# Optimization experiments

Hardware: AMD Instinct MI355X
Metric: run time of the kernel (lower is better)

The kernel has to match this reference:

```python
import jax, jax.numpy as jnp
import numpy as np
import itertools

RANK = 2  # window size per axis; mode='linear' -> stride 1; rank_op='avg'; rank_mode='drop'


def setup_inputs() -> dict:
    key = jax.random.key(0)
    k1, k2, k3 = jax.random.split(key, 3)
    m = 32
    D = 20
    hypervol = jax.random.normal(k1, (D, D, D, D, m), dtype=jnp.float32)
    # nn.Linear weight init U(-0.5, 0.5); P init U(-0.1, 0.1)
    M_w = jax.random.uniform(k2, (m, m), dtype=jnp.float32, minval=-0.5, maxval=0.5)
    P = jax.random.uniform(k3, (m, m), dtype=jnp.float32, minval=-0.1, maxval=0.1)
    return {"hypervol": hypervol, "M_w": M_w, "P": P}


def reference(hypervol, M_w, P):
    m = P.shape[0]
    D1, D2, D3, D4, _ = hypervol.shape
    o1, o2, o3, o4 = D1 - RANK + 1, D2 - RANK + 1, D3 - RANK + 1, D4 - RANK + 1

    # Vectorized window extraction with mean reduction ('avg'):
    # mean over RANK^4 window = average of RANK^4 shifted slices (fixed small loop).
    acc = jnp.zeros((o1, o2, o3, o4, m), dtype=hypervol.dtype)
    for a, b, c, d in itertools.product(range(RANK), repeat=4):
        acc = acc + hypervol[a:a + o1, b:b + o2, c:c + o3, d:d + o4, :]
    win = acc / float(RANK ** 4)  # [o1,o2,o3,o4,m]

    # M(v): Linear without bias -> v @ W^T
    x = jnp.einsum('abcdj,ij->abcdi', win, M_w)  # [o1,o2,o3,o4,m]
    # note: output index of Linear is i; below x plays role of (M v) with einsum index j
    x = jnp.einsum('abcdi->abcdi', x)  # no-op, keep shape clear

    # periods[i,j] = i*m + j + 2 (identical for all four axes)
    ii = jnp.arange(m, dtype=jnp.float32)
    periods = ii[:, None] * m + ii[None, :] + 2.0  # [m,m]
    two_pi = jnp.float32(2.0 * np.pi)

    def ctab(n):
        k = jnp.arange(n, dtype=jnp.float32)
        return jnp.cos(two_pi * k[:, None, None] / periods)  # [n,m,m]

    C1, C2, C3, C4 = ctab(o1), ctab(o2), ctab(o3), ctab(o4)
    # phi[a,b,c,d,i,j] = C1[a]*C2[b]*C3[c]*C4[d]; built from tiny per-axis tables
    phi = (C1[:, None, None, None] * C2[None, :, None, None]) \
          [:, :, :, None] * 0.0  # placeholder removed below
    phi = (C1[:, None, None, None, :, :]
           * C2[None, :, None, None, :, :]
           * C3[None, None, :, None, :, :]
           * C4[None, None, None, :, :, :])  # [o1,o2,o3,o4,m,m]

    # N(k)_i = sum_j P_ij * (Mv)_j * phi_ij  (matches einsum 'bj,ij,bij->bi')
    Nk = jnp.einsum('abcdj,ij,abcdij->abcdi', x, P, phi)
    return Nk.reshape(-1, m)  # [num_windows, m], window order = k1-major like the loops
```

## Files before the change

### kernel.cpp

```cpp
#include <hip/hip_runtime.h>

#define DD 20
#define MM 32
#define OO 19
#define NWIN (OO*OO*OO)
#define WPB 4
#define NBLK ((NWIN + WPB - 1) / WPB)

#define CT_FLOATS (OO*MM*MM)
#define PT_OFF CT_FLOATS
#define MT_OFF (PT_OFF + MM*MM)
#define WS_FLOATS (MT_OFF + MM*MM)

__global__ __launch_bounds__(256) void build_tables_kernel(
        const float* __restrict__ Mw, const float* __restrict__ P,
        float* __restrict__ ws) {
    int idx = blockIdx.x * 256 + threadIdx.x;
    if (idx < CT_FLOATS) {
        int k = idx >> 10;
        int r = idx & 1023;
        int j = r >> 5;
        int i = r & 31;
        float period = (float)(i * MM + j + 2);
        ws[idx] = cosf(6.28318530717958647692f * (float)k / period);
    } else if (idx < MT_OFF) {
        int r = idx - PT_OFF;
        ws[idx] = P[(r & 31) * MM + (r >> 5)];
    } else if (idx < WS_FLOATS) {
        int r = idx - MT_OFF;
        ws[idx] = Mw[(r & 31) * MM + (r >> 5)];
    }
}

__device__ __forceinline__ void wave_sync() {
    __builtin_amdgcn_s_waitcnt(0);
    __builtin_amdgcn_wave_barrier();
}

__global__ __launch_bounds__(256, 4) void spatial_kernel(
        const float* __restrict__ H, const float* __restrict__ ws,
        float* __restrict__ out) {
    __shared__ __align__(16) float sS[WPB][DD * MM];
    __shared__ __align__(16) float sW[WPB][OO * MM];
    __shared__ __align__(16) float sX[WPB][OO * MM];

    const int tid  = threadIdx.x;
    const int w    = tid >> 6;
    const int lane = tid & 63;
    const int i    = lane & 31;
    const int h    = lane >> 5;
    const int jb   = h * 16;

    const int raw = blockIdx.x;
    const int xcd = raw & 7;
    const int k   = raw >> 3;
    const int sb  = (xcd < 3) ? (xcd * 215 + k) : (645 + (xcd - 3) * 214 + k);
    const int win = sb * WPB + w;
    if (win >= NWIN) return;
    const int c = win % OO;
    const int b = (win / OO) % OO;
    const int a = win / (OO * OO);

    const float* __restrict__ Ct = ws;
    const float* __restrict__ Pt = ws + PT_OFF;
    const float* __restrict__ Mt = ws + MT_OFF;

    float* __restrict__ S = sS[w];
    float* __restrict__ W = sW[w];
    float* __restrict__ X = sX[w];

    {
        float2 acc[5];
        #pragma unroll
        for (int kk = 0; kk < 5; ++kk) acc[kk] = make_float2(0.f, 0.f);
        #pragma unroll
        for (int da = 0; da < 2; ++da)
            #pragma unroll
            for (int db = 0; db < 2; ++db)
                #pragma unroll
                for (int dc = 0; dc < 2; ++dc) {
                    const float2* __restrict__ p = (const float2*)(
                        H + (size_t)((((a + da) * DD + (b + db)) * DD + (c + dc)) * DD) * MM);
                    #pragma unroll
                    for (int kk = 0; kk < 5; ++kk) {
                        const float2 v = p[kk * 64 + lane];
                        acc[kk].x += v.x; acc[kk].y += v.y;
                    }
                }
        #pragma unroll
        for (int kk = 0; kk < 5; ++kk)
            ((float2*)S)[kk * 64 + lane] = acc[kk];
    }
    wave_sync();

    #pragma unroll
    for (int t = 0; t < 10; ++t) {
        const int idx = t * 64 + lane;
        if (idx < OO * MM)
            W[idx] = (S[idx] + S[idx + MM]) * 0.0625f;
    }
    wave_sync();

    {
        float mt[16];
        #pragma unroll
        for (int jj = 0; jj < 16; ++jj)
            mt[jj] = Mt[(jb + jj) * MM + i];

        #pragma unroll
        for (int d = 0; d < OO; ++d) {
            const float4* __restrict__ wr = (const float4*)(W + d * MM + jb);
            float t = 0.f;
            #pragma unroll
            for (int q = 0; q < 4; ++q) {
                const float4 v = wr[q];
                t += v.x * mt[q*4+0] + v.y * mt[q*4+1]
                   + v.z * mt[q*4+2] + v.w * mt[q*4+3];
            }
            t += __shfl_xor(t, 32, 64);
            if (h == 0) X[d * MM + i] = t;
        }
    }
    wave_sync();

    float s0[16], s1[16], t2c[16];
    {
        const float* __restrict__ cta = Ct + a * (MM * MM);
        const float* __restrict__ ctb = Ct + b * (MM * MM);
        const float* __restrict__ ctc = Ct + c * (MM * MM);
        const float* __restrict__ ct1 = Ct + 1 * (MM * MM);
        #pragma unroll
        for (int jj = 0; jj < 16; ++jj) {
            const int o = (jb + jj) * MM + i;
            const float qp  = Pt[o] * cta[o] * ctb[o] * ctc[o];
            const float cw  = ct1[o];
            t2c[jj] = cw + cw;
            s1[jj]  = qp;
            s0[jj]  = qp * cw;
        }
    }
    const size_t obase = (size_t)win * (OO * MM);
    #pragma unroll
    for (int d = 0; d < OO; ++d) {
        const float4* __restrict__ xr = (const float4*)(X + d * MM + jb);
        float t = 0.f;
        #pragma unroll
        for (int q = 0; q < 4; ++q) {
            const float4 v = xr[q];
            t += v.x * s1[q*4+0] + v.y * s1[q*4+1]
               + v.z * s1[q*4+2] + v.w * s1[q*4+3];
        }
        #pragma unroll
        for (int jj = 0; jj < 16; ++jj) {
            const float nx = __builtin_fmaf(t2c[jj], s1[jj], -s0[jj]);
            s0[jj] = s1[jj];
            s1[jj] = nx;
        }
        t += __shfl_xor(t, 32, 64);
        if (h == 0) out[obase + d * MM + i] = t;
    }
}

extern "C" void kernel_launch(void* const* d_in, const int* in_sizes, int n_in,
                              void* d_out, int out_size, void* d_ws, size_t ws_size,
                              hipStream_t stream) {
    const float* H  = (const float*)d_in[0];
    const float* Mw = (const float*)d_in[1];
    const float* P  = (const float*)d_in[2];
    float* out = (float*)d_out;
    float* ws  = (float*)d_ws;

    const int tblocks = (WS_FLOATS + 255) / 256;
    build_tables_kernel<<<tblocks, 256, 0, stream>>>(Mw, P, ws);
    spatial_kernel<<<NBLK, 256, 0, stream>>>(H, ws, out);
}
```

Baseline: 94.78 us.

## Split spatial kernel into two stages with global intermediate and vectorized loads

Splits the fused kernel into stage1 (window averaging plus the M projection, written to a global workspace) and stage2 (the cosine-recurrence contraction with P, read back from global). Each stage uses less LDS and fewer registers, so more waves can be resident per CU. The cos table layout is transposed so P, M and the tables are read with contiguous float4 loads directly instead of through pre-transposed copies. The price is an extra kernel launch and an intermediate array of about 26 MB written and read through global memory, and the LDS sync now waits only on LDS counters.

Result: slower. 134.3 us (+41.8%).

```diff
diff --git a/kernel.cpp b/kernel.cpp
--- a/kernel.cpp
+++ b/kernel.cpp
@@ -8,41 +8,38 @@
 #define NBLK ((NWIN + WPB - 1) / WPB)
 
 #define CT_FLOATS (OO*MM*MM)
-#define PT_OFF CT_FLOATS
-#define MT_OFF (PT_OFF + MM*MM)
-#define WS_FLOATS (MT_OFF + MM*MM)
+#define XOFF CT_FLOATS
+#define XROW (OO*MM)
 
-__global__ __launch_bounds__(256) void build_tables_kernel(
-        const float* __restrict__ Mw, const float* __restrict__ P,
-        float* __restrict__ ws) {
+__global__ __launch_bounds__(256) void build_tables_kernel(float* __restrict__ ws) {
     int idx = blockIdx.x * 256 + threadIdx.x;
     if (idx < CT_FLOATS) {
         int k = idx >> 10;
         int r = idx & 1023;
-        int j = r >> 5;
-        int i = r & 31;
+        int i = r >> 5;
+        int j = r & 31;
         float period = (float)(i * MM + j + 2);
         ws[idx] = cosf(6.28318530717958647692f * (float)k / period);
-    } else if (idx < MT_OFF) {
-        int r = idx - PT_OFF;
-        ws[idx] = P[(r & 31) * MM + (r >> 5)];
-    } else if (idx < WS_FLOATS) {
-        int r = idx - MT_OFF;
-        ws[idx] = Mw[(r & 31) * MM + (r >> 5)];
     }
 }
 
-__device__ __forceinline__ void wave_sync() {
-    __builtin_amdgcn_s_waitcnt(0);
+__device__ __forceinline__ void lds_sync() {
+    __builtin_amdgcn_s_waitcnt(0xC07F);
     __builtin_amdgcn_wave_barrier();
 }
 
-__global__ __launch_bounds__(256, 4) void spatial_kernel(
-        const float* __restrict__ H, const float* __restrict__ ws,
-        float* __restrict__ out) {
+__device__ __forceinline__ int swizzled_win(int raw, int w) {
+    const int xcd = raw & 7;
+    const int k   = raw >> 3;
+    const int sb  = (xcd < 3) ? (xcd * 215 + k) : (645 + (xcd - 3) * 214 + k);
+    return sb * WPB + w;
+}
+
+__global__ __launch_bounds__(256, 8) void stage1_kernel(
+        const float* __restrict__ H, const float* __restrict__ Mw,
+        float* __restrict__ ws) {
     __shared__ __align__(16) float sS[WPB][DD * MM];
     __shared__ __align__(16) float sW[WPB][OO * MM];
-    __shared__ __align__(16) float sX[WPB][OO * MM];
 
     const int tid  = threadIdx.x;
     const int w    = tid >> 6;
@@ -51,47 +48,40 @@
     const int h    = lane >> 5;
     const int jb   = h * 16;
 
-    const int raw = blockIdx.x;
-    const int xcd = raw & 7;
-    const int k   = raw >> 3;
-    const int sb  = (xcd < 3) ? (xcd * 215 + k) : (645 + (xcd - 3) * 214 + k);
-    const int win = sb * WPB + w;
+    const int win = swizzled_win(blockIdx.x, w);
     if (win >= NWIN) return;
     const int c = win % OO;
     const int b = (win / OO) % OO;
     const int a = win / (OO * OO);
 
-    const float* __restrict__ Ct = ws;
-    const float* __restrict__ Pt = ws + PT_OFF;
-    const float* __restrict__ Mt = ws + MT_OFF;
-
     float* __restrict__ S = sS[w];
     float* __restrict__ W = sW[w];
-    float* __restrict__ X = sX[w];
 
     {
-        float2 acc[5];
-        #pragma unroll
-        for (int kk = 0; kk < 5; ++kk) acc[kk] = make_float2(0.f, 0.f);
+        float4 a0 = make_float4(0.f,0.f,0.f,0.f);
+        float4 a1 = a0, a2 = a0;
         #pragma unroll
         for (int da = 0; da < 2; ++da)
             #pragma unroll
             for (int db = 0; db < 2; ++db)
                 #pragma unroll
                 for (int dc = 0; dc < 2; ++dc) {
-                    const float2* __restrict__ p = (const float2*)(
+                    const float4* __restrict__ p = (const float4*)(
                         H + (size_t)((((a + da) * DD + (b + db)) * DD + (c + dc)) * DD) * MM);
-                    #pragma unroll
-                    for (int kk = 0; kk < 5; ++kk) {
-                        const float2 v = p[kk * 64 + lane];
-                        acc[kk].x += v.x; acc[kk].y += v.y;
+                    float4 v0 = p[lane];
+                    float4 v1 = p[64 + lane];
+                    a0.x += v0.x; a0.y += v0.y; a0.z += v0.z; a0.w += v0.w;
+                    a1.x += v1.x; a1.y += v1.y; a1.z += v1.z; a1.w += v1.w;
+                    if (lane < 32) {
+                        float4 v2 = p[128 + lane];
+                        a2.x += v2.x; a2.y += v2.y; a2.z += v2.z; a2.w += v2.w;
                     }
                 }
-        #pragma unroll
-        for (int kk = 0; kk < 5; ++kk)
-            ((float2*)S)[kk * 64 + lane] = acc[kk];
+        ((float4*)S)[lane]      = a0;
+        ((float4*)S)[64 + lane] = a1;
+        if (lane < 32) ((float4*)S)[128 + lane] = a2;
     }
-    wave_sync();
+    lds_sync();
 
     #pragma unroll
     for (int t = 0; t < 10; ++t) {
@@ -99,14 +89,16 @@
         if (idx < OO * MM)
             W[idx] = (S[idx] + S[idx + MM]) * 0.0625f;
     }
-    wave_sync();
+    lds_sync();
 
     {
         float mt[16];
         #pragma unroll
-        for (int jj = 0; jj < 16; ++jj)
-            mt[jj] = Mt[(jb + jj) * MM + i];
-
+        for (int q = 0; q < 4; ++q) {
+            const float4 v = ((const float4*)(Mw + i * MM + jb))[q];
+            mt[q*4+0] = v.x; mt[q*4+1] = v.y; mt[q*4+2] = v.z; mt[q*4+3] = v.w;
+        }
+        float* __restrict__ Xg = ws + XOFF + (size_t)win * XROW;
         #pragma unroll
         for (int d = 0; d < OO; ++d) {
             const float4* __restrict__ wr = (const float4*)(W + d * MM + jb);
@@ -118,35 +110,58 @@
                    + v.z * mt[q*4+2] + v.w * mt[q*4+3];
             }
             t += __shfl_xor(t, 32, 64);
-            if (h == 0) X[d * MM + i] = t;
+            if (h == 0) Xg[d * MM + i] = t;
         }
     }
-    wave_sync();
+}
+
+__global__ __launch_bounds__(256, 6) void stage2_kernel(
+        const float* __restrict__ ws, const float* __restrict__ P,
+        float* __restrict__ out) {
+    const int tid  = threadIdx.x;
+    const int w    = tid >> 6;
+    const int lane = tid & 63;
+    const int i    = lane & 31;
+    const int h    = lane >> 5;
+    const int jb   = h * 16;
+
+    const int win = swizzled_win(blockIdx.x, w);
+    if (win >= NWIN) return;
+    const int c = win % OO;
+    const int b = (win / OO) % OO;
+    const int a = win / (OO * OO);
+
+    const float* __restrict__ C = ws;
 
     float s0[16], s1[16], t2c[16];
     {
-        const float* __restrict__ cta = Ct + a * (MM * MM);
-        const float* __restrict__ ctb = Ct + b * (MM * MM);
-        const float* __restrict__ ctc = Ct + c * (MM * MM);
-        const float* __restrict__ ct1 = Ct + 1 * (MM * MM);
+        const int ro = i * MM + jb;
         #pragma unroll
-        for (int jj = 0; jj < 16; ++jj) {
-            const int o = (jb + jj) * MM + i;
-            const float qp  = Pt[o] * cta[o] * ctb[o] * ctc[o];
-            const float cw  = ct1[o];
-            t2c[jj] = cw + cw;
-            s1[jj]  = qp;
-            s0[jj]  = qp * cw;
+        for (int q = 0; q < 4; ++q) {
+            const float4 pv = ((const float4*)(P + ro))[q];
+            const float4 va = ((const float4*)(C + a * (MM*MM) + ro))[q];
+            const float4 vb = ((const float4*)(C + b * (MM*MM) + ro))[q];
+            const float4 vc = ((const float4*)(C + c * (MM*MM) + ro))[q];
+            const float4 c1 = ((const float4*)(C + 1 * (MM*MM) + ro))[q];
+            const float qpx = pv.x * va.x * vb.x * vc.x;
+            const float qpy = pv.y * va.y * vb.y * vc.y;
+            const float qpz = pv.z * va.z * vb.z * vc.z;
+            const float qpw = pv.w * va.w * vb.w * vc.w;
+            s1[q*4+0] = qpx; s0[q*4+0] = qpx * c1.x; t2c[q*4+0] = c1.x + c1.x;
+            s1[q*4+1] = qpy; s0[q*4+1] = qpy * c1.y; t2c[q*4+1] = c1.y + c1.y;
+            s1[q*4+2] = qpz; s0[q*4+2] = qpz * c1.z; t2c[q*4+2] = c1.z + c1.z;
+            s1[q*4+3] = qpw; s0[q*4+3] = qpw * c1.w; t2c[q*4+3] = c1.w + c1.w;
         }
     }
-    const size_t obase = (size_t)win * (OO * MM);
+
+    const float* __restrict__ Xg = ws + XOFF + (size_t)win * XROW + jb;
+    const size_t obase = (size_t)win * XROW;
     #pragma unroll
     for (int d = 0; d < OO; ++d) {
-        const float4* __restrict__ xr = (const float4*)(X + d * MM + jb);
         float t = 0.f;
         #pragma unroll
         for (int q = 0; q < 4; ++q) {
-            const float4 v = xr[q];
+            const float4 v = ((const float4*)(Xg + d * MM))[q];
             t += v.x * s1[q*4+0] + v.y * s1[q*4+1]
                + v.z * s1[q*4+2] + v.w * s1[q*4+3];
         }
@@ -170,7 +185,7 @@
     float* out = (float*)d_out;
     float* ws  = (float*)d_ws;
 
-    const int tblocks = (WS_FLOATS + 255) / 256;
-    build_tables_kernel<<<tblocks, 256, 0, stream>>>(Mw, P, ws);
-    spatial_kernel<<<NBLK, 256, 0, stream>>>(H, ws, out);
+    build_tables_kernel<<<CT_FLOATS / 256, 256, 0, stream>>>(ws);
+    stage1_kernel<<<NBLK, 256, 0, stream>>>(H, Mw, ws);
+    stage2_kernel<<<NBLK, 256, 0, stream>>>(ws, P, out);
 }
```
